# Kernel optimization log

Measured on AMD Instinct MI355X. Metric: run time of the kernel, lower is better.

Reference implementation:

```python
import jax, jax.numpy as jnp
import numpy as np

D_MODEL = 1024
D_STATE = 16
D_CONV = 4
EXPAND = 2
D_INNER = EXPAND * D_MODEL
BATCH = 2
SEQLEN = 2048


def setup_inputs() -> dict:
    key = jax.random.key(0)
    ks = jax.random.split(key, 8)
    s = 0.02
    return {
        "x": jax.random.normal(ks[0], (BATCH, SEQLEN, D_MODEL), jnp.float32),
        "W_in": jax.random.normal(ks[1], (D_MODEL, 2 * D_INNER), jnp.float32) * s,
        "conv_w": jax.random.normal(ks[2], (D_INNER, D_CONV), jnp.float32) * s,
        "conv_b": jnp.zeros((D_INNER,), jnp.float32),
        "W_x": jax.random.normal(ks[3], (D_INNER, 2 * D_STATE), jnp.float32) * s,
        "W_dt": jax.random.normal(ks[4], (D_INNER, D_INNER), jnp.float32) * s,
        "b_dt": jnp.zeros((D_INNER,), jnp.float32),
        "A_log": jnp.log(jnp.tile(jnp.arange(1, D_STATE + 1, dtype=jnp.float32), (D_INNER, 1))),
        "D": jnp.ones((D_INNER,), jnp.float32),
        "W_out": jax.random.normal(ks[5], (D_INNER, D_MODEL), jnp.float32) * s,
    }


def _silu(x):
    return x * jax.nn.sigmoid(x)


def _causal_depthwise_conv(x, w, b):
    # x: (B, L, C); w: (C, K); b: (C,). Matches torch Conv1d(groups=C, padding=K-1)[..., :L].
    K = w.shape[1]
    L = x.shape[1]
    xp = jnp.pad(x, ((0, 0), (K - 1, 0), (0, 0)))
    out = b
    for k in range(K):  # K=4, tiny fixed loop over taps
        out = out + xp[:, k:k + L, :] * w[:, k]
    return out


def _selective_scan(u, dt, A, Bm, Cm, D):
    # u, dt: (B, L, d_inner); Bm, Cm: (B, L, d_state); A: (d_inner, d_state); D: (d_inner,)
    def step(h, xs):
        u_t, dt_t, b_t, c_t = xs  # (B,di), (B,di), (B,ds), (B,ds)
        dA = jnp.exp(dt_t[:, :, None] * A[None])            # (B, di, ds)
        h = dA * h + (dt_t * u_t)[:, :, None] * b_t[:, None, :]
        y = jnp.einsum('bds,bs->bd', h, c_t) + D * u_t
        return h, y

    h0 = jnp.zeros((u.shape[0],) + A.shape, u.dtype)
    xs = (u.swapaxes(0, 1), dt.swapaxes(0, 1), Bm.swapaxes(0, 1), Cm.swapaxes(0, 1))
    _, ys = jax.lax.scan(step, h0, xs)  # ys: (L, B, d_inner)
    return ys.swapaxes(0, 1)


def reference(x, W_in, conv_w, conv_b, W_x, W_dt, b_dt, A_log, D, W_out):
    xz = x @ W_in                                  # (B, L, 2*d_inner)
    xp, z = jnp.split(xz, 2, axis=-1)
    xc = _silu(_causal_depthwise_conv(xp, conv_w, conv_b))
    Bm, Cm = jnp.split(xc @ W_x, 2, axis=-1)       # each (B, L, d_state)
    dt = jax.nn.softplus(xc @ W_dt + b_dt)         # (B, L, d_inner)
    A = -jnp.exp(A_log)                            # (d_inner, d_state)
    y = _selective_scan(xc, dt, A, Bm, Cm, D)
    y = y * _silu(z)
    return y @ W_out  # dropout is identity in eval mode
```

## Files before the change

### kernel.cpp

```cpp
#include <hip/hip_runtime.h>
#include <hip/hip_bf16.h>
#include <cstdint>
#include <cstddef>

#define BB 2
#define LL 2048
#define DM 1024
#define DI 2048
#define DS 16
#define MM (BB*LL)
#define NCAT 2176
#define NC 32
#define LC (LL/NC)

typedef __attribute__((ext_vector_type(8))) short short8;
typedef __attribute__((ext_vector_type(4))) float f32x4;

__device__ __forceinline__ unsigned short f2bf(float f) {
  union { float f; unsigned int u; } x; x.f = f;
  unsigned int u = x.u;
  unsigned int r = (u + 0x7FFFu + ((u >> 16) & 1u)) >> 16;
  return (unsigned short)r;
}

__global__ __launch_bounds__(256) void cast_bf16_k(const float* __restrict__ in,
                                                   unsigned short* __restrict__ out, int n) {
  int i = (blockIdx.x * 256 + threadIdx.x) * 4;
  if (i < n) {
    float4 v = *(const float4*)&in[i];
    ushort4 o;
    o.x = f2bf(v.x); o.y = f2bf(v.y); o.z = f2bf(v.z); o.w = f2bf(v.w);
    *(ushort4*)&out[i] = o;
  }
}

__global__ __launch_bounds__(256) void transpose_cast_k(const float* __restrict__ W,
                                                        unsigned short* __restrict__ WT,
                                                        int R, int C) {
  __shared__ float tile[32][33];
  int c0 = blockIdx.x * 32;
  int r0 = blockIdx.y * 32;
  int tx = threadIdx.x;
  int ty = threadIdx.y;
#pragma unroll
  for (int i = 0; i < 4; ++i) {
    int r = r0 + ty + i * 8;
    tile[ty + i * 8][tx] = W[(size_t)r * C + c0 + tx];
  }
  __syncthreads();
#pragma unroll
  for (int i = 0; i < 4; ++i) {
    int c = c0 + ty + i * 8;
    WT[(size_t)c * R + r0 + tx] = f2bf(tile[tx][ty + i * 8]);
  }
}

#define BM 128
#define BN 128
#define BK 32
template <int MODE>
__global__ __launch_bounds__(256) void gemm_bt_k(const unsigned short* __restrict__ A,
                                                 const unsigned short* __restrict__ Bt,
                                                 float* __restrict__ C,
                                                 int M, int N, int K,
                                                 const float* __restrict__ bias,
                                                 float* __restrict__ C2, int nSplit) {
  __shared__ unsigned short As[3][BM * BK];
  __shared__ unsigned short Bs[3][BN * BK];
  const int tid  = threadIdx.x;
  const int lane = tid & 63;
  const int wv   = tid >> 6;
  const int nTilesN = N / BN;
  const int bm = (blockIdx.x / nTilesN) * BM;
  const int bn = (blockIdx.x % nTilesN) * BN;
  const int wr = wv >> 1, wc = wv & 1;

  const int chunk0 = wv;
  const int eidx0  = chunk0 * 64 + lane;
  const int row0   = eidx0 >> 2;
  const int col0   = (eidx0 & 3) * 8;
  const int chunk1 = wv + 4;
  const int eidx1  = chunk1 * 64 + lane;
  const int row1   = eidx1 >> 2;
  const int col1   = (eidx1 & 3) * 8;
  const unsigned short* gA0 = A  + (size_t)(bm + row0) * K + col0;
  const unsigned short* gB0 = Bt + (size_t)(bn + row0) * K + col0;
  const unsigned short* gA1 = A  + (size_t)(bm + row1) * K + col1;
  const unsigned short* gB1 = Bt + (size_t)(bn + row1) * K + col1;

#define STAGE(buf, k0)                                                              \
  do {                                                                              \
    __builtin_amdgcn_global_load_lds(                                               \
        (const __attribute__((address_space(1))) unsigned int*)(gA0 + (k0)),        \
        (__attribute__((address_space(3))) unsigned int*)&As[buf][chunk0 * 512],    \
        16, 0, 0);                                                                  \
    __builtin_amdgcn_global_load_lds(                                               \
        (const __attribute__((address_space(1))) unsigned int*)(gB0 + (k0)),        \
        (__attribute__((address_space(3))) unsigned int*)&Bs[buf][chunk0 * 512],    \
        16, 0, 0);                                                                  \
    __builtin_amdgcn_global_load_lds(                                               \
        (const __attribute__((address_space(1))) unsigned int*)(gA1 + (k0)),        \
        (__attribute__((address_space(3))) unsigned int*)&As[buf][chunk1 * 512],    \
        16, 0, 0);                                                                  \
    __builtin_amdgcn_global_load_lds(                                               \
        (const __attribute__((address_space(1))) unsigned int*)(gB1 + (k0)),        \
        (__attribute__((address_space(3))) unsigned int*)&Bs[buf][chunk1 * 512],    \
        16, 0, 0);                                                                  \
  } while (0)

  f32x4 acc[4][4] = {};

  const int nK = K / BK;
  STAGE(0, 0);
  int cur = 0;
  for (int kt = 0; kt < nK; ++kt) {
    int nxt = (cur == 2) ? 0 : cur + 1;
    if (kt + 1 < nK) {
      STAGE(nxt, (kt + 1) * BK);
      asm volatile("s_waitcnt vmcnt(4)" ::: "memory");
    } else {
      asm volatile("s_waitcnt vmcnt(0)" ::: "memory");
    }
    __builtin_amdgcn_s_barrier();
    __builtin_amdgcn_sched_barrier(0);

    short8 af[4], bf[4];
    const int kofs = (lane >> 4) * 8;
#pragma unroll
    for (int i = 0; i < 4; ++i) {
      int ar = wr * 64 + i * 16 + (lane & 15);
      af[i] = *(const short8*)&As[cur][ar * BK + kofs];
      int br = wc * 64 + i * 16 + (lane & 15);
      bf[i] = *(const short8*)&Bs[cur][br * BK + kofs];
    }
#pragma unroll
    for (int i = 0; i < 4; ++i)
#pragma unroll
      for (int j = 0; j < 4; ++j)
        acc[i][j] = __builtin_amdgcn_mfma_f32_16x16x32_bf16(af[i], bf[j], acc[i][j], 0, 0, 0);
    cur = nxt;
  }
#undef STAGE

  const int colBase = bn + wc * 64;
  const int rowBase = bm + wr * 64;
#pragma unroll
  for (int i = 0; i < 4; ++i) {
#pragma unroll
    for (int j = 0; j < 4; ++j) {
      int c = colBase + j * 16 + (lane & 15);
#pragma unroll
      for (int r4 = 0; r4 < 4; ++r4) {
        int rr = rowBase + i * 16 + (lane >> 4) * 4 + r4;
        float v = acc[i][j][r4];
        if (MODE == 0) {
          C[(size_t)rr * N + c] = v;
        } else {
          if (c < nSplit) {
            float t = v + bias[c];
            C[(size_t)rr * nSplit + c] = (t > 20.f) ? t : log1pf(expf(t));
          } else if (c < nSplit + 32) {
            C2[(size_t)rr * 32 + (c - nSplit)] = v;
          }
        }
      }
    }
  }
}

__global__ __launch_bounds__(256) void conv_silu_k(const float* __restrict__ xz,
                                                   const float* __restrict__ cw,
                                                   const float* __restrict__ cb,
                                                   float* __restrict__ xc,
                                                   unsigned short* __restrict__ xcb) {
  int idx = blockIdx.x * 256 + threadIdx.x;
  int i4  = idx * 4;
  int c4  = i4 & (DI - 1);
  int row = i4 >> 11;
  int t   = row & (LL - 1);
  size_t base = (size_t)row * 4096 + c4;
  float4 x3 = *(const float4*)&xz[base];
  float4 x2 = (t >= 1) ? *(const float4*)&xz[base - 4096]  : float4{0, 0, 0, 0};
  float4 x1 = (t >= 2) ? *(const float4*)&xz[base - 8192]  : float4{0, 0, 0, 0};
  float4 x0 = (t >= 3) ? *(const float4*)&xz[base - 12288] : float4{0, 0, 0, 0};
  float4 bias = *(const float4*)&cb[c4];
  float4 w[4];
#pragma unroll
  for (int j = 0; j < 4; ++j) w[j] = *(const float4*)&cw[(c4 + j) * 4];
  float vx3[4] = {x3.x, x3.y, x3.z, x3.w};
  float vx2[4] = {x2.x, x2.y, x2.z, x2.w};
  float vx1[4] = {x1.x, x1.y, x1.z, x1.w};
  float vx0[4] = {x0.x, x0.y, x0.z, x0.w};
  float vb[4]  = {bias.x, bias.y, bias.z, bias.w};
  float4 so;
  ushort4 sb;
  float res[4];
#pragma unroll
  for (int j = 0; j < 4; ++j) {
    float v = vb[j];
    v = fmaf(vx3[j], w[j].w, v);
    v = fmaf(vx2[j], w[j].z, v);
    v = fmaf(vx1[j], w[j].y, v);
    v = fmaf(vx0[j], w[j].x, v);
    res[j] = v / (1.f + expf(-v));
  }
  so.x = res[0]; so.y = res[1]; so.z = res[2]; so.w = res[3];
  sb.x = f2bf(res[0]); sb.y = f2bf(res[1]); sb.z = f2bf(res[2]); sb.w = f2bf(res[3]);
  *(float4*)&xc[i4] = so;
  *(ushort4*)&xcb[i4] = sb;
}

__global__ __launch_bounds__(256) void scan1_k(const float* __restrict__ dt,
                                               const float* __restrict__ u,
                                               const float* __restrict__ BC,
                                               const float* __restrict__ A_log,
                                               float* __restrict__ Pc,
                                               float* __restrict__ Sc) {
  int tid = threadIdx.x;
  int b   = blockIdx.y;
  int cg  = blockIdx.x / NC;
  int nc  = blockIdx.x % NC;
  int d   = cg * 256 + tid;
  float A2[DS], h[DS];
#pragma unroll
  for (int s4 = 0; s4 < DS; s4 += 4) {
    float4 av = *(const float4*)&A_log[d * DS + s4];
    A2[s4 + 0] = -expf(av.x) * 1.44269504f;
    A2[s4 + 1] = -expf(av.y) * 1.44269504f;
    A2[s4 + 2] = -expf(av.z) * 1.44269504f;
    A2[s4 + 3] = -expf(av.w) * 1.44269504f;
    h[s4] = 0.f; h[s4 + 1] = 0.f; h[s4 + 2] = 0.f; h[s4 + 3] = 0.f;
  }
  float Tsum = 0.f;
  const int t0 = nc * LC;
  const float* dtp = dt + ((size_t)b * LL + t0) * DI + d;
  const float* up  = u  + ((size_t)b * LL + t0) * DI + d;
  const float* bcp = BC + ((size_t)b * LL + t0) * 32;
  for (int t = 0; t < LC; ++t) {
    float dtv = dtp[(size_t)t * DI];
    float uv  = up[(size_t)t * DI];
    float dtu = dtv * uv;
    Tsum += dtv;
#pragma unroll
    for (int s = 0; s < DS; ++s) {
      float dA = exp2f(dtv * A2[s]);
      h[s] = fmaf(dA, h[s], dtu * bcp[t * 32 + s]);
    }
  }
  size_t o = (((size_t)b * NC + nc) * DI + d) * DS;
#pragma unroll
  for (int s4 = 0; s4 < DS; s4 += 4) {
    float4 pv = {exp2f(A2[s4] * Tsum), exp2f(A2[s4 + 1] * Tsum),
                 exp2f(A2[s4 + 2] * Tsum), exp2f(A2[s4 + 3] * Tsum)};
    *(float4*)&Pc[o + s4] = pv;
    float4 sv = {h[s4], h[s4 + 1], h[s4 + 2], h[s4 + 3]};
    *(float4*)&Sc[o + s4] = sv;
  }
}

__global__ __launch_bounds__(256) void scanmid_k(const float* __restrict__ Pc,
                                                 const float* __restrict__ Sc,
                                                 float* __restrict__ H0) {
  int idx = blockIdx.x * 256 + threadIdx.x;
  int b   = idx >> 15;
  int e   = idx & (DI * DS - 1);
  size_t base = ((size_t)b * NC) * DI * DS + e;
  float h = 0.f;
#pragma unroll
  for (int j = 0; j < NC; ++j) {
    size_t o = base + (size_t)j * DI * DS;
    H0[o] = h;
    h = fmaf(Pc[o], h, Sc[o]);
  }
}

__global__ __launch_bounds__(256) void scan2_k(const float* __restrict__ dt,
                                               const float* __restrict__ u,
                                               const float* __restrict__ BC,
                                               const float* __restrict__ xz,
                                               const float* __restrict__ A_log,
                                               const float* __restrict__ Dp,
                                               const float* __restrict__ H0,
                                               unsigned short* __restrict__ ymb) {
  int tid = threadIdx.x;
  int b   = blockIdx.y;
  int cg  = blockIdx.x / NC;
  int nc  = blockIdx.x % NC;
  int d   = cg * 256 + tid;
  float A2[DS], h[DS];
  size_t hb = (((size_t)b * NC + nc) * DI + d) * DS;
#pragma unroll
  for (int s4 = 0; s4 < DS; s4 += 4) {
    float4 av = *(const float4*)&A_log[d * DS + s4];
    A2[s4 + 0] = -expf(av.x) * 1.44269504f;
    A2[s4 + 1] = -expf(av.y) * 1.44269504f;
    A2[s4 + 2] = -expf(av.z) * 1.44269504f;
    A2[s4 + 3] = -expf(av.w) * 1.44269504f;
    float4 hv = *(const float4*)&H0[hb + s4];
    h[s4] = hv.x; h[s4 + 1] = hv.y; h[s4 + 2] = hv.z; h[s4 + 3] = hv.w;
  }
  float Dd = Dp[d];
  const int t0 = nc * LC;
  const float* dtp = dt + ((size_t)b * LL + t0) * DI + d;
  const float* up  = u  + ((size_t)b * LL + t0) * DI + d;
  const float* bcp = BC + ((size_t)b * LL + t0) * 32;
  const float* zp  = xz + ((size_t)b * LL + t0) * 4096 + DI + d;
  unsigned short* yp = ymb + ((size_t)b * LL + t0) * DI + d;
  for (int t = 0; t < LC; ++t) {
    float dtv = dtp[(size_t)t * DI];
    float uv  = up[(size_t)t * DI];
    float dtu = dtv * uv;
    float y   = 0.f;
#pragma unroll
    for (int s = 0; s < DS; ++s) {
      float dA = exp2f(dtv * A2[s]);
      h[s] = fmaf(dA, h[s], dtu * bcp[t * 32 + s]);
      y = fmaf(h[s], bcp[t * 32 + 16 + s], y);
    }
    float zv = zp[(size_t)t * 4096];
    y = fmaf(Dd, uv, y);
    float sz = zv / (1.f + expf(-zv));
    yp[(size_t)t * DI] = f2bf(y * sz);
  }
}

extern "C" void kernel_launch(void* const* d_in, const int* in_sizes, int n_in,
                              void* d_out, int out_size, void* d_ws, size_t ws_size,
                              hipStream_t stream) {
  const float* x      = (const float*)d_in[0];
  const float* W_in   = (const float*)d_in[1];
  const float* conv_w = (const float*)d_in[2];
  const float* conv_b = (const float*)d_in[3];
  const float* W_x    = (const float*)d_in[4];
  const float* W_dt   = (const float*)d_in[5];
  const float* b_dt   = (const float*)d_in[6];
  const float* A_log  = (const float*)d_in[7];
  const float* Dv     = (const float*)d_in[8];
  const float* W_out  = (const float*)d_in[9];
  float* out = (float*)d_out;

  char* w = (char*)d_ws;
  float* xz  = (float*)w;            w += (size_t)MM * 4096 * 4;
  float* xc  = (float*)w;            w += (size_t)MM * DI * 4;
  float* dtb = (float*)w;            w += (size_t)MM * DI * 4;
  float* BC  = (float*)w;            w += (size_t)MM * 32 * 4;
  float* Pc  = (float*)w;            w += (size_t)BB * NC * DI * DS * 4;
  float* Sc  = (float*)w;            w += (size_t)BB * NC * DI * DS * 4;
  float* H0  = (float*)w;            w += (size_t)BB * NC * DI * DS * 4;
  unsigned short* x_b   = (unsigned short*)w; w += (size_t)MM * DM * 2;
  unsigned short* xc_b  = (unsigned short*)w; w += (size_t)MM * DI * 2;
  unsigned short* ym_b  = (unsigned short*)w; w += (size_t)MM * DI * 2;
  unsigned short* WinT  = (unsigned short*)w; w += (size_t)(2 * DI) * DM * 2;
  unsigned short* WcatT = (unsigned short*)w; w += (size_t)NCAT * DI * 2;
  unsigned short* WoutT = (unsigned short*)w; w += (size_t)DM * DI * 2;

  cast_bf16_k<<<(MM * DM) / 1024, 256, 0, stream>>>(x, x_b, MM * DM);
  transpose_cast_k<<<dim3(4096 / 32, DM / 32), dim3(32, 8), 0, stream>>>(W_in, WinT, DM, 4096);
  transpose_cast_k<<<dim3(DI / 32, DI / 32), dim3(32, 8), 0, stream>>>(W_dt, WcatT, DI, DI);
  transpose_cast_k<<<dim3(1, DI / 32), dim3(32, 8), 0, stream>>>(W_x, WcatT + (size_t)DI * DI, DI, 32);
  hipMemsetAsync(WcatT + (size_t)(DI + 32) * DI, 0, (size_t)(NCAT - DI - 32) * DI * 2, stream);
  transpose_cast_k<<<dim3(DM / 32, DI / 32), dim3(32, 8), 0, stream>>>(W_out, WoutT, DI, DM);

  gemm_bt_k<0><<<(MM / BM) * (4096 / BN), 256, 0, stream>>>(x_b, WinT, xz, MM, 4096, DM,
                                                            nullptr, nullptr, 0);
  conv_silu_k<<<(MM * DI) / 1024, 256, 0, stream>>>(xz, conv_w, conv_b, xc, xc_b);

  gemm_bt_k<1><<<(MM / BM) * (NCAT / BN), 256, 0, stream>>>(xc_b, WcatT, dtb, MM, NCAT, DI,
                                                            b_dt, BC, DI);
  scan1_k<<<dim3((DI / 256) * NC, BB), 256, 0, stream>>>(dtb, xc, BC, A_log, Pc, Sc);
  scanmid_k<<<(BB * DI * DS) / 256, 256, 0, stream>>>(Pc, Sc, H0);
  scan2_k<<<dim3((DI / 256) * NC, BB), 256, 0, stream>>>(dtb, xc, BC, xz, A_log, Dv, H0, ym_b);

  gemm_bt_k<0><<<(MM / BM) * (DM / BN), 256, 0, stream>>>(ym_b, WoutT, out, MM, DM, DI,
                                                          nullptr, nullptr, 0);
}
```

Measured before the change: 462.2 us.

## Add 256x256-tile 8-wave bf16 GEMM with 4-stage pipeline for input and dt projections

```diff
diff --git a/kernel.cpp b/kernel.cpp
--- a/kernel.cpp
+++ b/kernel.cpp
@@ -9,7 +9,7 @@
 #define DI 2048
 #define DS 16
 #define MM (BB*LL)
-#define NCAT 2176
+#define NCAT2 2304
 #define NC 32
 #define LC (LL/NC)
 
@@ -52,6 +52,120 @@
   for (int i = 0; i < 4; ++i) {
     int c = c0 + ty + i * 8;
     WT[(size_t)c * R + r0 + tx] = f2bf(tile[tx][ty + i * 8]);
+  }
+}
+
+template <int MODE>
+__global__ __launch_bounds__(512, 2) void gemm256_k(const unsigned short* __restrict__ A,
+                                                    const unsigned short* __restrict__ Bt,
+                                                    float* __restrict__ C,
+                                                    int M, int N, int K,
+                                                    const float* __restrict__ bias,
+                                                    float* __restrict__ C2, int nSplit) {
+  __shared__ unsigned short Asl[4][256 * 32];
+  __shared__ unsigned short Bsl[4][256 * 32];
+  const int tid  = threadIdx.x;
+  const int lane = tid & 63;
+  const int wid  = tid >> 6;
+  const int wr   = wid >> 2;
+  const int wcn  = wid & 3;
+  const int nTilesN = N / 256;
+  const int bm = (blockIdx.x / nTilesN) * 256;
+  const int bn = (blockIdx.x % nTilesN) * 256;
+
+  const int srow = tid >> 2;
+  const int scol = (((tid & 3) ^ ((tid >> 3) & 3)) << 3);
+  const unsigned short* gA = A  + (size_t)(bm + srow) * K + scol;
+  const unsigned short* gB = Bt + (size_t)(bn + srow) * K + scol;
+  const size_t gStep = (size_t)128 * K;
+
+  const int kswz = (((lane >> 4) ^ ((lane >> 1) & 3)) << 3);
+  const int arow = wr * 128 + (lane & 15);
+  const int brow = wcn * 64 + (lane & 15);
+
+  f32x4 acc[8][4] = {};
+  const int nT = K / 32;
+
+#define STG(dst, src, k0, shot)                                                               \
+    __builtin_amdgcn_global_load_lds(                                                         \
+        (const __attribute__((address_space(1))) unsigned int*)((src) + (k0) + (shot) * gStep), \
+        (__attribute__((address_space(3))) unsigned int*)&(dst)[(shot) * 4096 + (wid << 9)],  \
+        16, 0, 0)
+
+  STG(Asl[0], gA, 0, 0);  STG(Asl[0], gA, 0, 1);
+  STG(Bsl[0], gB, 0, 0);  STG(Bsl[0], gB, 0, 1);
+  STG(Asl[1], gA, 32, 0); STG(Asl[1], gA, 32, 1);
+  STG(Bsl[1], gB, 32, 0); STG(Bsl[1], gB, 32, 1);
+  asm volatile("s_waitcnt vmcnt(4)" ::: "memory");
+  __builtin_amdgcn_s_barrier();
+
+  for (int t = 0; t < nT; ++t) {
+    const int rb = t & 3;
+    const int sb = (t + 2) & 3;
+    const int k2 = (t + 2) * 32;
+    const bool more = (t + 2) < nT;
+    short8 af[8], bf[4];
+    if (more) { STG(Asl[sb], gA, k2, 0); STG(Asl[sb], gA, k2, 1); }
+#pragma unroll
+    for (int i = 0; i < 8; ++i)
+      af[i] = *(const short8*)&Asl[rb][(arow + i * 16) * 32 + kswz];
+#pragma unroll
+    for (int j = 0; j < 2; ++j)
+      bf[j] = *(const short8*)&Bsl[rb][(brow + j * 16) * 32 + kswz];
+    asm volatile("s_waitcnt lgkmcnt(0)" ::: "memory");
+    __builtin_amdgcn_sched_barrier(0);
+    __builtin_amdgcn_s_barrier();
+    __builtin_amdgcn_s_setprio(1);
+#pragma unroll
+    for (int i = 0; i < 8; ++i) {
+      acc[i][0] = __builtin_amdgcn_mfma_f32_16x16x32_bf16(af[i], bf[0], acc[i][0], 0, 0, 0);
+      acc[i][1] = __builtin_amdgcn_mfma_f32_16x16x32_bf16(af[i], bf[1], acc[i][1], 0, 0, 0);
+    }
+    __builtin_amdgcn_s_setprio(0);
+    __builtin_amdgcn_s_barrier();
+    if (more) { STG(Bsl[sb], gB, k2, 0); STG(Bsl[sb], gB, k2, 1); }
+#pragma unroll
+    for (int j = 2; j < 4; ++j)
+      bf[j] = *(const short8*)&Bsl[rb][(brow + j * 16) * 32 + kswz];
+    asm volatile("s_waitcnt lgkmcnt(0)" ::: "memory");
+    __builtin_amdgcn_sched_barrier(0);
+    __builtin_amdgcn_s_barrier();
+    __builtin_amdgcn_s_setprio(1);
+#pragma unroll
+    for (int i = 0; i < 8; ++i) {
+      acc[i][2] = __builtin_amdgcn_mfma_f32_16x16x32_bf16(af[i], bf[2], acc[i][2], 0, 0, 0);
+      acc[i][3] = __builtin_amdgcn_mfma_f32_16x16x32_bf16(af[i], bf[3], acc[i][3], 0, 0, 0);
+    }
+    __builtin_amdgcn_s_setprio(0);
+    if (more) asm volatile("s_waitcnt vmcnt(4)" ::: "memory");
+    else      asm volatile("s_waitcnt vmcnt(0)" ::: "memory");
+    __builtin_amdgcn_s_barrier();
+  }
+#undef STG
+
+  const int colBase = bn + wcn * 64;
+  const int rowBase = bm + wr * 128;
+#pragma unroll
+  for (int i = 0; i < 8; ++i) {
+#pragma unroll
+    for (int j = 0; j < 4; ++j) {
+      int c = colBase + j * 16 + (lane & 15);
+#pragma unroll
+      for (int r4 = 0; r4 < 4; ++r4) {
+        int rr = rowBase + i * 16 + (lane >> 4) * 4 + r4;
+        float v = acc[i][j][r4];
+        if (MODE == 0) {
+          C[(size_t)rr * N + c] = v;
+        } else {
+          if (c < nSplit) {
+            float tv = v + bias[c];
+            C[(size_t)rr * nSplit + c] = (tv > 20.f) ? tv : log1pf(expf(tv));
+          } else if (c < nSplit + 32) {
+            C2[(size_t)rr * 32 + (c - nSplit)] = v;
+          }
+        }
+      }
+    }
   }
 }
 
@@ -109,7 +223,6 @@
   } while (0)
 
   f32x4 acc[4][4] = {};
-
   const int nK = K / BK;
   STAGE(0, 0);
   int cur = 0;
@@ -351,22 +464,21 @@
   unsigned short* xc_b  = (unsigned short*)w; w += (size_t)MM * DI * 2;
   unsigned short* ym_b  = (unsigned short*)w; w += (size_t)MM * DI * 2;
   unsigned short* WinT  = (unsigned short*)w; w += (size_t)(2 * DI) * DM * 2;
-  unsigned short* WcatT = (unsigned short*)w; w += (size_t)NCAT * DI * 2;
+  unsigned short* WcatT = (unsigned short*)w; w += (size_t)NCAT2 * DI * 2;
   unsigned short* WoutT = (unsigned short*)w; w += (size_t)DM * DI * 2;
 
   cast_bf16_k<<<(MM * DM) / 1024, 256, 0, stream>>>(x, x_b, MM * DM);
   transpose_cast_k<<<dim3(4096 / 32, DM / 32), dim3(32, 8), 0, stream>>>(W_in, WinT, DM, 4096);
   transpose_cast_k<<<dim3(DI / 32, DI / 32), dim3(32, 8), 0, stream>>>(W_dt, WcatT, DI, DI);
   transpose_cast_k<<<dim3(1, DI / 32), dim3(32, 8), 0, stream>>>(W_x, WcatT + (size_t)DI * DI, DI, 32);
-  hipMemsetAsync(WcatT + (size_t)(DI + 32) * DI, 0, (size_t)(NCAT - DI - 32) * DI * 2, stream);
   transpose_cast_k<<<dim3(DM / 32, DI / 32), dim3(32, 8), 0, stream>>>(W_out, WoutT, DI, DM);
 
-  gemm_bt_k<0><<<(MM / BM) * (4096 / BN), 256, 0, stream>>>(x_b, WinT, xz, MM, 4096, DM,
-                                                            nullptr, nullptr, 0);
+  gemm256_k<0><<<(MM / 256) * (4096 / 256), 512, 0, stream>>>(x_b, WinT, xz, MM, 4096, DM,
+                                                              nullptr, nullptr, 0);
   conv_silu_k<<<(MM * DI) / 1024, 256, 0, stream>>>(xz, conv_w, conv_b, xc, xc_b);
 
-  gemm_bt_k<1><<<(MM / BM) * (NCAT / BN), 256, 0, stream>>>(xc_b, WcatT, dtb, MM, NCAT, DI,
-                                                            b_dt, BC, DI);
+  gemm256_k<1><<<(MM / 256) * (NCAT2 / 256), 512, 0, stream>>>(xc_b, WcatT, dtb, MM, NCAT2, DI,
+                                                               b_dt, BC, DI);
   scan1_k<<<dim3((DI / 256) * NC, BB), 256, 0, stream>>>(dtb, xc, BC, A_log, Pc, Sc);
   scanmid_k<<<(BB * DI * DS) / 256, 256, 0, stream>>>(Pc, Sc, H0);
   scan2_k<<<dim3((DI / 256) * NC, BB), 256, 0, stream>>>(dtb, xc, BC, xz, A_log, Dv, H0, ym_b);
```

Result: slower. 526.9 us (+14.0%).
